# Optimization experiments

Measured on AMD Instinct MI355X. Metric: run time of the kernel, lower is better.

Reference implementation:

```python
import jax, jax.numpy as jnp
import numpy as np

ENC_DIM, DEC_DIM, ATT_DIM = 2048, 512, 512

def setup_inputs() -> dict:
    key = jax.random.key(0)
    ks = jax.random.split(key, 8)
    s_enc = 1.0 / np.sqrt(ENC_DIM)
    s_dec = 1.0 / np.sqrt(DEC_DIM)
    s_att = 1.0 / np.sqrt(ATT_DIM)
    return {
        "encoder_out": jax.random.normal(ks[0], (256, 196, ENC_DIM), jnp.float32),
        "decoder_hidden": jax.random.normal(ks[1], (256, DEC_DIM), jnp.float32),
        "W_enc": jax.random.uniform(ks[2], (ENC_DIM, ATT_DIM), jnp.float32, -s_enc, s_enc),
        "b_enc": jax.random.uniform(ks[3], (ATT_DIM,), jnp.float32, -s_enc, s_enc),
        "W_dec": jax.random.uniform(ks[4], (DEC_DIM, ATT_DIM), jnp.float32, -s_dec, s_dec),
        "b_dec": jax.random.uniform(ks[5], (ATT_DIM,), jnp.float32, -s_dec, s_dec),
        "W_att": jax.random.uniform(ks[6], (ATT_DIM, 1), jnp.float32, -s_att, s_att),
        "b_att": jax.random.uniform(ks[7], (1,), jnp.float32, -s_att, s_att),
    }

def reference(encoder_out, decoder_hidden, W_enc, b_enc, W_dec, b_dec, W_att, b_att):
    # att1: (B, P, A); att2: (B, 1, A)
    att1 = jnp.einsum('bpe,ea->bpa', encoder_out, W_enc) + b_enc
    att2 = (decoder_hidden @ W_dec + b_dec)[:, None, :]
    # scalar score per pixel: (B, P)
    e = (jax.nn.relu(att1 + att2) @ W_att)[..., 0] + b_att[0]
    alpha = jax.nn.softmax(e, axis=-1)  # softmax over pixels
    z = jnp.einsum('bpe,bp->be', encoder_out, alpha)
    return (z, alpha)
```

## Files before the change

### kernel.cpp

```cpp
#include <hip/hip_runtime.h>
#include <hip/hip_bf16.h>

#define ENC_DIM 2048
#define DEC_DIM 512
#define ATT_DIM 512
#define NB 256
#define NP 196
#define M_TOT (NB * NP)
#define BM 64
#define BK 32
#define NSTEP (ENC_DIM / BK)

typedef __attribute__((ext_vector_type(8))) short short8;
typedef __attribute__((ext_vector_type(4))) float f32x4;

__device__ __forceinline__ short8 cvt8v(f32x4 x, f32x4 y) {
    union { short8 v; __hip_bfloat16 h[8]; } u;
    u.h[0] = __float2bfloat16(x[0]);
    u.h[1] = __float2bfloat16(x[1]);
    u.h[2] = __float2bfloat16(x[2]);
    u.h[3] = __float2bfloat16(x[3]);
    u.h[4] = __float2bfloat16(y[0]);
    u.h[5] = __float2bfloat16(y[1]);
    u.h[6] = __float2bfloat16(y[2]);
    u.h[7] = __float2bfloat16(y[3]);
    return u.v;
}

__global__ __launch_bounds__(256) void prep_kernel(const float* __restrict__ W,
                                                   __hip_bfloat16* __restrict__ Btt,
                                                   const float* __restrict__ dec,
                                                   const float* __restrict__ W_dec,
                                                   const float* __restrict__ b_dec,
                                                   const float* __restrict__ b_enc,
                                                   float* __restrict__ att2f) {
    __shared__ float ds[DEC_DIM];
    if (blockIdx.x < 512) {
        const int gid = blockIdx.x * 256 + threadIdx.x;
        const int s   = gid >> 11;
        const int u   = gid & 2047;
        const int fr  = u >> 6;
        const int kg  = (u >> 4) & 3;
        const int l15 = u & 15;
        const int col = fr * 16 + l15;
        const int k0  = s * 32 + kg * 8;
        union { short8 v; __hip_bfloat16 h[8]; } x;
        #pragma unroll
        for (int i = 0; i < 8; ++i)
            x.h[i] = __float2bfloat16(W[(size_t)(k0 + i) * ATT_DIM + col]);
        *(short8*)((short*)Btt + (size_t)gid * 8) = x.v;
    } else {
        const int b = blockIdx.x - 512;
        const int t = threadIdx.x;
        ds[t]       = dec[(size_t)b * DEC_DIM + t];
        ds[t + 256] = dec[(size_t)b * DEC_DIM + t + 256];
        __syncthreads();
        #pragma unroll
        for (int j = 0; j < 2; ++j) {
            const int n = t + j * 256;
            float s = 0.f;
            #pragma unroll 8
            for (int k = 0; k < DEC_DIM; ++k)
                s += ds[k] * W_dec[(size_t)k * ATT_DIM + n];
            att2f[(size_t)b * ATT_DIM + n] = s + b_dec[n] + b_enc[n];
        }
    }
}

__global__ __launch_bounds__(512, 2) void e_kernel(const float* __restrict__ enc,
                                                   const short* __restrict__ Btt,
                                                   const float* __restrict__ att2f,
                                                   const float* __restrict__ W_att,
                                                   float* __restrict__ e_out) {
    __shared__ __attribute__((aligned(16))) short As[32 * 256 * 8];
    __shared__ float ebuf[8][64];

    const int tid  = threadIdx.x;
    const int lane = tid & 63;
    const int wv   = tid >> 6;
    const int l15  = lane & 15;
    const int kg   = lane >> 4;
    const int M0   = blockIdx.x * BM;

    const int srow = tid >> 3;
    const int sc   = tid & 7;
    const float* sbase = enc + (size_t)(M0 + srow) * ENC_DIM + sc * 8;
    const int wbase = (((sc >> 2) * 256) + ((srow >> 4) * 64) + ((sc & 3) * 16) + (srow & 15)) * 8;

    const short* pBb = Btt + wv * 2048 + kg * 128 + l15 * 8;

    f32x4 acc[4][4];
    #pragma unroll
    for (int i = 0; i < 4; ++i)
        #pragma unroll
        for (int j = 0; j < 4; ++j)
            acc[i][j] = (f32x4){0.f, 0.f, 0.f, 0.f};

#define MFMA16(A0, A1, A2, A3, B0, B1, B2, B3)                                       \
    acc[0][0] = __builtin_amdgcn_mfma_f32_16x16x32_bf16(A0, B0, acc[0][0], 0, 0, 0); \
    acc[0][1] = __builtin_amdgcn_mfma_f32_16x16x32_bf16(A0, B1, acc[0][1], 0, 0, 0); \
    acc[0][2] = __builtin_amdgcn_mfma_f32_16x16x32_bf16(A0, B2, acc[0][2], 0, 0, 0); \
    acc[0][3] = __builtin_amdgcn_mfma_f32_16x16x32_bf16(A0, B3, acc[0][3], 0, 0, 0); \
    acc[1][0] = __builtin_amdgcn_mfma_f32_16x16x32_bf16(A1, B0, acc[1][0], 0, 0, 0); \
    acc[1][1] = __builtin_amdgcn_mfma_f32_16x16x32_bf16(A1, B1, acc[1][1], 0, 0, 0); \
    acc[1][2] = __builtin_amdgcn_mfma_f32_16x16x32_bf16(A1, B2, acc[1][2], 0, 0, 0); \
    acc[1][3] = __builtin_amdgcn_mfma_f32_16x16x32_bf16(A1, B3, acc[1][3], 0, 0, 0); \
    acc[2][0] = __builtin_amdgcn_mfma_f32_16x16x32_bf16(A2, B0, acc[2][0], 0, 0, 0); \
    acc[2][1] = __builtin_amdgcn_mfma_f32_16x16x32_bf16(A2, B1, acc[2][1], 0, 0, 0); \
    acc[2][2] = __builtin_amdgcn_mfma_f32_16x16x32_bf16(A2, B2, acc[2][2], 0, 0, 0); \
    acc[2][3] = __builtin_amdgcn_mfma_f32_16x16x32_bf16(A2, B3, acc[2][3], 0, 0, 0); \
    acc[3][0] = __builtin_amdgcn_mfma_f32_16x16x32_bf16(A3, B0, acc[3][0], 0, 0, 0); \
    acc[3][1] = __builtin_amdgcn_mfma_f32_16x16x32_bf16(A3, B1, acc[3][1], 0, 0, 0); \
    acc[3][2] = __builtin_amdgcn_mfma_f32_16x16x32_bf16(A3, B2, acc[3][2], 0, 0, 0); \
    acc[3][3] = __builtin_amdgcn_mfma_f32_16x16x32_bf16(A3, B3, acc[3][3], 0, 0, 0);

    for (int p = 0; p < 2; ++p) {
        __syncthreads();
        {
            const float* sp = sbase + (size_t)p * 1024;
            #pragma unroll
            for (int i = 0; i < 16; ++i) {
                f32x4 lo = *(const f32x4*)(sp + i * 64);
                f32x4 hi = *(const f32x4*)(sp + i * 64 + 4);
                *(short8*)&As[wbase + i * 4096] = cvt8v(lo, hi);
            }
        }
        __syncthreads();

        const int S0 = p * 32;
        const short* pb0 = pBb + (size_t)S0 * 16384;
        short8 c0 = *(const short8*)(pb0);
        short8 c1 = *(const short8*)(pb0 + 512);
        short8 c2 = *(const short8*)(pb0 + 1024);
        short8 c3 = *(const short8*)(pb0 + 1536);
        short8 n0, n1, n2, n3;

        for (int s = 0; s < 32; s += 2) {
            {
                const short* p1 = pBb + (size_t)(S0 + s + 1) * 16384;
                n0 = *(const short8*)(p1);
                n1 = *(const short8*)(p1 + 512);
                n2 = *(const short8*)(p1 + 1024);
                n3 = *(const short8*)(p1 + 1536);
                __builtin_amdgcn_sched_barrier(0);
                const short* Ab = &As[s * 2048];
                const short8 a0 = *(const short8*)&Ab[0 * 512 + lane * 8];
                const short8 a1 = *(const short8*)&Ab[1 * 512 + lane * 8];
                const short8 a2 = *(const short8*)&Ab[2 * 512 + lane * 8];
                const short8 a3 = *(const short8*)&Ab[3 * 512 + lane * 8];
                __builtin_amdgcn_s_setprio(1);
                MFMA16(a0, a1, a2, a3, c0, c1, c2, c3)
                __builtin_amdgcn_s_setprio(0);
            }
            {
                const short* p2 = pBb + (size_t)((S0 + s + 2) & 63) * 16384;
                c0 = *(const short8*)(p2);
                c1 = *(const short8*)(p2 + 512);
                c2 = *(const short8*)(p2 + 1024);
                c3 = *(const short8*)(p2 + 1536);
                __builtin_amdgcn_sched_barrier(0);
                const short* Ab = &As[(s + 1) * 2048];
                const short8 a0 = *(const short8*)&Ab[0 * 512 + lane * 8];
                const short8 a1 = *(const short8*)&Ab[1 * 512 + lane * 8];
                const short8 a2 = *(const short8*)&Ab[2 * 512 + lane * 8];
                const short8 a3 = *(const short8*)&Ab[3 * 512 + lane * 8];
                __builtin_amdgcn_s_setprio(1);
                MFMA16(a0, a1, a2, a3, n0, n1, n2, n3)
                __builtin_amdgcn_s_setprio(0);
            }
        }
    }
#undef MFMA16

    float wat[4];
    #pragma unroll
    for (int nf = 0; nf < 4; ++nf) wat[nf] = W_att[wv * 64 + nf * 16 + l15];

    #pragma unroll
    for (int mf = 0; mf < 4; ++mf) {
        #pragma unroll
        for (int rr = 0; rr < 4; ++rr) {
            const int ml = mf * 16 + kg * 4 + rr;
            const int bb = (M0 + ml) / NP;
            const float* arow2 = att2f + (size_t)bb * ATT_DIM + wv * 64 + l15;
            float sv = 0.f;
            #pragma unroll
            for (int nf = 0; nf < 4; ++nf) {
                float v = acc[mf][nf][rr] + arow2[nf * 16];
                sv += fmaxf(v, 0.f) * wat[nf];
            }
            sv += __shfl_xor(sv, 1);
            sv += __shfl_xor(sv, 2);
            sv += __shfl_xor(sv, 4);
            sv += __shfl_xor(sv, 8);
            if (l15 == 0) ebuf[wv][ml] = sv;
        }
    }
    __syncthreads();
    if (tid < 64) {
        float sv = 0.f;
        #pragma unroll
        for (int w = 0; w < 8; ++w) sv += ebuf[w][tid];
        e_out[M0 + tid] = sv;
    }
}

__global__ __launch_bounds__(256) void z_kernel(const float* __restrict__ enc,
                                                const float* __restrict__ e,
                                                float* __restrict__ z,
                                                float* __restrict__ alpha) {
    const int b  = blockIdx.x;
    const int cb = blockIdx.y;
    const int t  = threadIdx.x;
    __shared__ float al[NP];
    __shared__ float red[4];

    float ev = (t < NP) ? e[(size_t)b * NP + t] : -1e30f;
    float m = ev;
    #pragma unroll
    for (int o = 32; o > 0; o >>= 1) m = fmaxf(m, __shfl_xor(m, o));
    if ((t & 63) == 0) red[t >> 6] = m;
    __syncthreads();
    m = fmaxf(fmaxf(red[0], red[1]), fmaxf(red[2], red[3]));
    __syncthreads();
    float ex = (t < NP) ? __expf(ev - m) : 0.f;
    float s = ex;
    #pragma unroll
    for (int o = 32; o > 0; o >>= 1) s += __shfl_xor(s, o);
    if ((t & 63) == 0) red[t >> 6] = s;
    __syncthreads();
    s = red[0] + red[1] + red[2] + red[3];
    const float a = ex * (1.0f / s);
    if (t < NP) {
        al[t] = a;
        if (cb == 0) alpha[(size_t)b * NP + t] = a;
    }
    __syncthreads();

    const int c0 = cb * 1024 + t * 4;
    const float4* ep = (const float4*)(enc + (size_t)b * NP * ENC_DIM + c0);
    float4 z0 = make_float4(0.f, 0.f, 0.f, 0.f);
    float4 z1 = make_float4(0.f, 0.f, 0.f, 0.f);
    #pragma unroll 4
    for (int p = 0; p < NP; p += 2) {
        const float a0 = al[p];
        const float a1 = al[p + 1];
        const float4 v0 = ep[(size_t)p * (ENC_DIM / 4)];
        const float4 v1 = ep[(size_t)(p + 1) * (ENC_DIM / 4)];
        z0.x += a0 * v0.x; z0.y += a0 * v0.y; z0.z += a0 * v0.z; z0.w += a0 * v0.w;
        z1.x += a1 * v1.x; z1.y += a1 * v1.y; z1.z += a1 * v1.z; z1.w += a1 * v1.w;
    }
    z0.x += z1.x; z0.y += z1.y; z0.z += z1.z; z0.w += z1.w;
    *(float4*)(z + (size_t)b * ENC_DIM + c0) = z0;
}

extern "C" void kernel_launch(void* const* d_in, const int* in_sizes, int n_in,
                              void* d_out, int out_size, void* d_ws, size_t ws_size,
                              hipStream_t stream) {
    const float* enc   = (const float*)d_in[0];
    const float* dec   = (const float*)d_in[1];
    const float* W_enc = (const float*)d_in[2];
    const float* b_enc = (const float*)d_in[3];
    const float* W_dec = (const float*)d_in[4];
    const float* b_dec = (const float*)d_in[5];
    const float* W_att = (const float*)d_in[6];

    float* z     = (float*)d_out;
    float* alpha = z + (size_t)NB * ENC_DIM;

    char* ws = (char*)d_ws;
    __hip_bfloat16* Btt = (__hip_bfloat16*)ws;
    float* att2f        = (float*)(ws + 2 * 1024 * 1024);
    float* e            = (float*)(ws + 2 * 1024 * 1024 + 512 * 1024);

    prep_kernel<<<768, 256, 0, stream>>>(W_enc, Btt, dec, W_dec, b_dec, b_enc, att2f);
    e_kernel<<<M_TOT / BM, 512, 0, stream>>>(enc, (const short*)Btt, att2f, W_att, e);
    z_kernel<<<dim3(NB, 2), 256, 0, stream>>>(enc, e, z, alpha);
}
```

Measured before the change: 299.1 us.

## Retile e_kernel to 128-row, N-split tiles with double-buffered pipelined A staging

Each e_kernel block now handles a 128-row M tile and one half of the 512 attention columns, and the grid is grouped so that 8 M tiles share each N half. The A operand is streamed from global memory one K-step at a time into a double-buffered 8 KB LDS tile, with prefetch overlapped with the MFMAs, instead of converting the whole 64x2048 slab into a large LDS buffer up front. Partial scores for the two N halves go to separate buffers and are summed in z_kernel. This cuts LDS footprint and the up-front load stall, which should allow better occupancy and overlap. In exchange, each encoder row is read twice (once per N half) and there is a barrier every K-step.

```diff
diff --git a/kernel.cpp b/kernel.cpp
--- a/kernel.cpp
+++ b/kernel.cpp
@@ -7,7 +7,7 @@
 #define NB 256
 #define NP 196
 #define M_TOT (NB * NP)
-#define BM 64
+#define BM 128
 #define BK 32
 #define NSTEP (ENC_DIM / BK)
 
@@ -71,124 +71,109 @@
                                                    const short* __restrict__ Btt,
                                                    const float* __restrict__ att2f,
                                                    const float* __restrict__ W_att,
-                                                   float* __restrict__ e_out) {
-    __shared__ __attribute__((aligned(16))) short As[32 * 256 * 8];
-    __shared__ float ebuf[8][64];
+                                                   float* __restrict__ e_part) {
+    __shared__ __attribute__((aligned(16))) short As[2][4096];
+    __shared__ float ebuf[8][128];
 
     const int tid  = threadIdx.x;
     const int lane = tid & 63;
     const int wv   = tid >> 6;
     const int l15  = lane & 15;
     const int kg   = lane >> 4;
-    const int M0   = blockIdx.x * BM;
-
-    const int srow = tid >> 3;
-    const int sc   = tid & 7;
-    const float* sbase = enc + (size_t)(M0 + srow) * ENC_DIM + sc * 8;
-    const int wbase = (((sc >> 2) * 256) + ((srow >> 4) * 64) + ((sc & 3) * 16) + (srow & 15)) * 8;
-
-    const short* pBb = Btt + wv * 2048 + kg * 128 + l15 * 8;
-
-    f32x4 acc[4][4];
-    #pragma unroll
-    for (int i = 0; i < 4; ++i)
-        #pragma unroll
-        for (int j = 0; j < 4; ++j)
-            acc[i][j] = (f32x4){0.f, 0.f, 0.f, 0.f};
-
-#define MFMA16(A0, A1, A2, A3, B0, B1, B2, B3)                                       \
-    acc[0][0] = __builtin_amdgcn_mfma_f32_16x16x32_bf16(A0, B0, acc[0][0], 0, 0, 0); \
-    acc[0][1] = __builtin_amdgcn_mfma_f32_16x16x32_bf16(A0, B1, acc[0][1], 0, 0, 0); \
-    acc[0][2] = __builtin_amdgcn_mfma_f32_16x16x32_bf16(A0, B2, acc[0][2], 0, 0, 0); \
-    acc[0][3] = __builtin_amdgcn_mfma_f32_16x16x32_bf16(A0, B3, acc[0][3], 0, 0, 0); \
-    acc[1][0] = __builtin_amdgcn_mfma_f32_16x16x32_bf16(A1, B0, acc[1][0], 0, 0, 0); \
-    acc[1][1] = __builtin_amdgcn_mfma_f32_16x16x32_bf16(A1, B1, acc[1][1], 0, 0, 0); \
-    acc[1][2] = __builtin_amdgcn_mfma_f32_16x16x32_bf16(A1, B2, acc[1][2], 0, 0, 0); \
-    acc[1][3] = __builtin_amdgcn_mfma_f32_16x16x32_bf16(A1, B3, acc[1][3], 0, 0, 0); \
-    acc[2][0] = __builtin_amdgcn_mfma_f32_16x16x32_bf16(A2, B0, acc[2][0], 0, 0, 0); \
-    acc[2][1] = __builtin_amdgcn_mfma_f32_16x16x32_bf16(A2, B1, acc[2][1], 0, 0, 0); \
-    acc[2][2] = __builtin_amdgcn_mfma_f32_16x16x32_bf16(A2, B2, acc[2][2], 0, 0, 0); \
-    acc[2][3] = __builtin_amdgcn_mfma_f32_16x16x32_bf16(A2, B3, acc[2][3], 0, 0, 0); \
-    acc[3][0] = __builtin_amdgcn_mfma_f32_16x16x32_bf16(A3, B0, acc[3][0], 0, 0, 0); \
-    acc[3][1] = __builtin_amdgcn_mfma_f32_16x16x32_bf16(A3, B1, acc[3][1], 0, 0, 0); \
-    acc[3][2] = __builtin_amdgcn_mfma_f32_16x16x32_bf16(A3, B2, acc[3][2], 0, 0, 0); \
-    acc[3][3] = __builtin_amdgcn_mfma_f32_16x16x32_bf16(A3, B3, acc[3][3], 0, 0, 0);
-
-    for (int p = 0; p < 2; ++p) {
-        __syncthreads();
+
+    const int bid = blockIdx.x;
+    const int g   = bid >> 4;
+    const int r   = bid & 15;
+    const int nh  = r >> 3;
+    const int mt  = g * 8 + (r & 7);
+    const int M0  = mt * BM;
+    const int N0  = nh * 256;
+
+    const int srow = tid >> 2;
+    const int sc   = tid & 3;
+    const float* asrc = enc + (size_t)(M0 + srow) * ENC_DIM + sc * 8;
+    const int awr = (srow >> 4) * 512 + sc * 128 + (srow & 15) * 8;
+
+    const short* pBb = Btt + (nh * 16 + wv * 2) * 512 + kg * 128 + l15 * 8;
+
+    f32x4 acc[8][2];
+    #pragma unroll
+    for (int i = 0; i < 8; ++i) {
+        acc[i][0] = (f32x4){0.f, 0.f, 0.f, 0.f};
+        acc[i][1] = (f32x4){0.f, 0.f, 0.f, 0.f};
+    }
+
+#define MFMA_STEP(BUF, B0, B1)                                                           \
+    {                                                                                    \
+        const short* Ab = &As[BUF][0];                                                   \
+        _Pragma("unroll")                                                                \
+        for (int mf = 0; mf < 8; ++mf) {                                                 \
+            const short8 a = *(const short8*)&Ab[mf * 512 + lane * 8];                   \
+            acc[mf][0] = __builtin_amdgcn_mfma_f32_16x16x32_bf16(a, B0, acc[mf][0], 0, 0, 0); \
+            acc[mf][1] = __builtin_amdgcn_mfma_f32_16x16x32_bf16(a, B1, acc[mf][1], 0, 0, 0); \
+        }                                                                                \
+    }
+
+    {
+        f32x4 lo = *(const f32x4*)asrc;
+        f32x4 hi = *(const f32x4*)(asrc + 4);
+        *(short8*)&As[0][awr] = cvt8v(lo, hi);
+    }
+    f32x4 avPa = *(const f32x4*)(asrc + BK);
+    f32x4 avPb = *(const f32x4*)(asrc + BK + 4);
+    short8 c0 = *(const short8*)(pBb);
+    short8 c1 = *(const short8*)(pBb + 512);
+    short8 n0, n1;
+    asm volatile("s_waitcnt lgkmcnt(0)" ::: "memory");
+    __builtin_amdgcn_s_barrier();
+
+    for (int s = 0; s < NSTEP; s += 2) {
         {
-            const float* sp = sbase + (size_t)p * 1024;
-            #pragma unroll
-            for (int i = 0; i < 16; ++i) {
-                f32x4 lo = *(const f32x4*)(sp + i * 64);
-                f32x4 hi = *(const f32x4*)(sp + i * 64 + 4);
-                *(short8*)&As[wbase + i * 4096] = cvt8v(lo, hi);
-            }
-        }
-        __syncthreads();
-
-        const int S0 = p * 32;
-        const short* pb0 = pBb + (size_t)S0 * 16384;
-        short8 c0 = *(const short8*)(pb0);
-        short8 c1 = *(const short8*)(pb0 + 512);
-        short8 c2 = *(const short8*)(pb0 + 1024);
-        short8 c3 = *(const short8*)(pb0 + 1536);
-        short8 n0, n1, n2, n3;
-
-        for (int s = 0; s < 32; s += 2) {
-            {
-                const short* p1 = pBb + (size_t)(S0 + s + 1) * 16384;
-                n0 = *(const short8*)(p1);
-                n1 = *(const short8*)(p1 + 512);
-                n2 = *(const short8*)(p1 + 1024);
-                n3 = *(const short8*)(p1 + 1536);
-                __builtin_amdgcn_sched_barrier(0);
-                const short* Ab = &As[s * 2048];
-                const short8 a0 = *(const short8*)&Ab[0 * 512 + lane * 8];
-                const short8 a1 = *(const short8*)&Ab[1 * 512 + lane * 8];
-                const short8 a2 = *(const short8*)&Ab[2 * 512 + lane * 8];
-                const short8 a3 = *(const short8*)&Ab[3 * 512 + lane * 8];
-                __builtin_amdgcn_s_setprio(1);
-                MFMA16(a0, a1, a2, a3, c0, c1, c2, c3)
-                __builtin_amdgcn_s_setprio(0);
-            }
-            {
-                const short* p2 = pBb + (size_t)((S0 + s + 2) & 63) * 16384;
-                c0 = *(const short8*)(p2);
-                c1 = *(const short8*)(p2 + 512);
-                c2 = *(const short8*)(p2 + 1024);
-                c3 = *(const short8*)(p2 + 1536);
-                __builtin_amdgcn_sched_barrier(0);
-                const short* Ab = &As[(s + 1) * 2048];
-                const short8 a0 = *(const short8*)&Ab[0 * 512 + lane * 8];
-                const short8 a1 = *(const short8*)&Ab[1 * 512 + lane * 8];
-                const short8 a2 = *(const short8*)&Ab[2 * 512 + lane * 8];
-                const short8 a3 = *(const short8*)&Ab[3 * 512 + lane * 8];
-                __builtin_amdgcn_s_setprio(1);
-                MFMA16(a0, a1, a2, a3, n0, n1, n2, n3)
-                __builtin_amdgcn_s_setprio(0);
-            }
-        }
-    }
-#undef MFMA16
-
-    float wat[4];
-    #pragma unroll
-    for (int nf = 0; nf < 4; ++nf) wat[nf] = W_att[wv * 64 + nf * 16 + l15];
-
-    #pragma unroll
-    for (int mf = 0; mf < 4; ++mf) {
+            const short* p1 = pBb + (size_t)(s + 1) * 16384;
+            n0 = *(const short8*)(p1);
+            n1 = *(const short8*)(p1 + 512);
+            f32x4 avNa = *(const f32x4*)(asrc + (size_t)((s + 2) & 63) * BK);
+            f32x4 avNb = *(const f32x4*)(asrc + (size_t)((s + 2) & 63) * BK + 4);
+            __builtin_amdgcn_sched_barrier(0);
+            __builtin_amdgcn_s_setprio(1);
+            MFMA_STEP(0, c0, c1)
+            __builtin_amdgcn_s_setprio(0);
+            *(short8*)&As[1][awr] = cvt8v(avPa, avPb);
+            avPa = avNa; avPb = avNb;
+            asm volatile("s_waitcnt lgkmcnt(0)" ::: "memory");
+            __builtin_amdgcn_s_barrier();
+        }
+        {
+            const short* p2 = pBb + (size_t)((s + 2) & 63) * 16384;
+            c0 = *(const short8*)(p2);
+            c1 = *(const short8*)(p2 + 512);
+            f32x4 avNa = *(const f32x4*)(asrc + (size_t)((s + 3) & 63) * BK);
+            f32x4 avNb = *(const f32x4*)(asrc + (size_t)((s + 3) & 63) * BK + 4);
+            __builtin_amdgcn_sched_barrier(0);
+            __builtin_amdgcn_s_setprio(1);
+            MFMA_STEP(1, n0, n1)
+            __builtin_amdgcn_s_setprio(0);
+            *(short8*)&As[0][awr] = cvt8v(avPa, avPb);
+            avPa = avNa; avPb = avNb;
+            asm volatile("s_waitcnt lgkmcnt(0)" ::: "memory");
+            __builtin_amdgcn_s_barrier();
+        }
+    }
+#undef MFMA_STEP
+
+    float wat[2];
+    wat[0] = W_att[N0 + wv * 32 + l15];
+    wat[1] = W_att[N0 + wv * 32 + 16 + l15];
+
+    #pragma unroll
+    for (int mf = 0; mf < 8; ++mf) {
         #pragma unroll
         for (int rr = 0; rr < 4; ++rr) {
             const int ml = mf * 16 + kg * 4 + rr;
             const int bb = (M0 + ml) / NP;
-            const float* arow2 = att2f + (size_t)bb * ATT_DIM + wv * 64 + l15;
-            float sv = 0.f;
-            #pragma unroll
-            for (int nf = 0; nf < 4; ++nf) {
-                float v = acc[mf][nf][rr] + arow2[nf * 16];
-                sv += fmaxf(v, 0.f) * wat[nf];
-            }
+            const float* arow2 = att2f + (size_t)bb * ATT_DIM + N0 + wv * 32 + l15;
+            float sv = fmaxf(acc[mf][0][rr] + arow2[0], 0.f) * wat[0] +
+                       fmaxf(acc[mf][1][rr] + arow2[16], 0.f) * wat[1];
             sv += __shfl_xor(sv, 1);
             sv += __shfl_xor(sv, 2);
             sv += __shfl_xor(sv, 4);
@@ -197,16 +182,16 @@
         }
     }
     __syncthreads();
-    if (tid < 64) {
+    if (tid < 128) {
         float sv = 0.f;
         #pragma unroll
         for (int w = 0; w < 8; ++w) sv += ebuf[w][tid];
-        e_out[M0 + tid] = sv;
+        e_part[(size_t)nh * M_TOT + M0 + tid] = sv;
     }
 }
 
 __global__ __launch_bounds__(256) void z_kernel(const float* __restrict__ enc,
-                                                const float* __restrict__ e,
+                                                const float* __restrict__ e_part,
                                                 float* __restrict__ z,
                                                 float* __restrict__ alpha) {
     const int b  = blockIdx.x;
@@ -215,7 +200,9 @@
     __shared__ float al[NP];
     __shared__ float red[4];
 
-    float ev = (t < NP) ? e[(size_t)b * NP + t] : -1e30f;
+    float ev = -1e30f;
+    if (t < NP)
+        ev = e_part[(size_t)b * NP + t] + e_part[(size_t)M_TOT + b * NP + t];
     float m = ev;
     #pragma unroll
     for (int o = 32; o > 0; o >>= 1) m = fmaxf(m, __shfl_xor(m, o));
@@ -271,9 +258,9 @@
     char* ws = (char*)d_ws;
     __hip_bfloat16* Btt = (__hip_bfloat16*)ws;
     float* att2f        = (float*)(ws + 2 * 1024 * 1024);
-    float* e            = (float*)(ws + 2 * 1024 * 1024 + 512 * 1024);
+    float* e_part       = (float*)(ws + 2 * 1024 * 1024 + 512 * 1024);
 
     prep_kernel<<<768, 256, 0, stream>>>(W_enc, Btt, dec, W_dec, b_dec, b_enc, att2f);
-    e_kernel<<<M_TOT / BM, 512, 0, stream>>>(enc, (const short*)Btt, att2f, W_att, e);
-    z_kernel<<<dim3(NB, 2), 256, 0, stream>>>(enc, e, z, alpha);
-}
+    e_kernel<<<(M_TOT / BM) * 2, 512, 0, stream>>>(enc, (const short*)Btt, att2f, W_att, e_part);
+    z_kernel<<<dim3(NB, 2), 256, 0, stream>>>(enc, e_part, z, alpha);
+}
```

Measured after the change: 293.2 us. Within noise of the previous version (-2.0%).
